# Optimization experiments

Hardware: AMD Instinct MI355X
Metric: run time of the kernel (lower is better)

## Reference

```python
import jax, jax.numpy as jnp
import numpy as np

B, C, H, W = 32, 128, 56, 56
O = 256
KH, KW = 3, 3
SH, SW = 1, 1
PH, PW = 1, 1
T = 6          # num_terms
R = 8          # low_rank
D = C * KH * KW          # 1152
R2 = R * KH * KW         # 72


def setup_inputs() -> dict:
    key = jax.random.key(0)
    ks = jax.random.split(key, 6)
    scale = 0.05
    return {
        "x": jax.random.normal(ks[0], (B, C, H, W), dtype=jnp.float32),
        "S1s": jax.random.normal(ks[1], (T, D, R), dtype=jnp.float32) * scale,
        "U1s": jax.random.normal(ks[2], (T, R, O), dtype=jnp.float32) * scale,
        "U2s": jax.random.normal(ks[3], (T, R2, D), dtype=jnp.float32) * scale,
        "S2s": jax.random.normal(ks[4], (T, R2, O), dtype=jnp.float32) * scale,
        "bias": jax.random.normal(ks[5], (O,), dtype=jnp.float32) * scale,
    }


def _extract_windows(x):
    # im2col: pad then gather strided windows; d flattened in (C, kh, kw) order
    xp = jnp.pad(x, ((0, 0), (0, 0), (PH, PH), (PW, PW)))
    Hp, Wp = xp.shape[2], xp.shape[3]
    Ho = (Hp - KH) // SH + 1
    Wo = (Wp - KW) // SW + 1
    # stack KH*KW shifted views -> [B, C, KH*KW, Ho, Wo]
    patches = jnp.stack(
        [xp[:, :, i:i + SH * Ho:SH, j:j + SW * Wo:SW]
         for i in range(KH) for j in range(KW)],
        axis=2,
    )
    # -> [B, Ho, Wo, C, KH*KW] -> [N, C*KH*KW]
    xw = patches.transpose(0, 3, 4, 1, 2).reshape(B * Ho * Wo, D)
    return xw, Ho, Wo


def reference(x, S1s, U1s, U2s, S2s, bias):
    xw, Ho, Wo = _extract_windows(x)                    # [N, D]
    # term 1: x_windows @ S1s[t] @ U1s[t], averaged over terms
    out1 = jnp.einsum('nd,tdr,tro->no', xw, S1s, U1s, optimize=True) / T + bias
    # term 2: x_windows @ U2s[t].T @ S2s[t], averaged over terms
    out2 = jnp.einsum('nd,tdr,tro->no', xw, jnp.swapaxes(U2s, 1, 2), S2s,
                      optimize=True) / T
    # NOTE: bias is added twice, faithfully matching the original module
    out = (out1 + out2 + bias).reshape(B, Ho, Wo, O).transpose(0, 3, 1, 2)
    return out
```

## Files before the change

### kernel.cpp

```cpp
#include <hip/hip_runtime.h>
#include <hip/hip_bf16.h>

typedef __attribute__((ext_vector_type(8))) short  short8;
typedef __attribute__((ext_vector_type(8))) unsigned short ushort8;
typedef __attribute__((ext_vector_type(4))) unsigned short usv4;
typedef __attribute__((ext_vector_type(4))) float  f32x4;

#define D_DIM 1152
#define O_DIM 256
#define N_TOT 100352
#define XT_H 58
#define XT_ROW (58 * 128)

__device__ __forceinline__ unsigned short f2bf(float f) {
  __hip_bfloat16 h = __float2bfloat16(f);
  return __builtin_bit_cast(unsigned short, h);
}

#define GLOAD_LDS16(g, l)                                              \
  __builtin_amdgcn_global_load_lds(                                    \
      (const __attribute__((address_space(1))) void*)(g),              \
      (__attribute__((address_space(3))) void*)(l), 16, 0, 0)

__global__ __launch_bounds__(256) void wt_kernel(
    const float* __restrict__ S1s, const float* __restrict__ U1s,
    const float* __restrict__ U2s, const float* __restrict__ S2s,
    unsigned short* __restrict__ Wt) {
  __shared__ float A_lds[32][64];
  __shared__ float B_lds[32][64];

  const int bo = blockIdx.x & 3;
  const int bd = blockIdx.x >> 2;
  const int o0  = bo << 6;
  const int dn0 = bd << 6;
  const int rr  = dn0 >> 7;
  const int c0  = dn0 & 127;

  const int tid = threadIdx.x;
  const int ty = tid >> 4, tx = tid & 15;

  float acc[4][4] = {};

  for (int kc = 0; kc < 15; ++kc) {
#pragma unroll
    for (int e = 0; e < 8; ++e) {
      const int li = e * 256 + tid;
      const int kk = li >> 6;
      const int xx = li & 63;
      const int k  = kc * 32 + kk;
      float av, bv;
      if (k < 48) {
        av = U1s[k * O_DIM + o0 + xx];
        const int d_old = (c0 + xx) * 9 + rr;
        bv = S1s[(size_t)((k >> 3) * D_DIM + d_old) * 8 + (k & 7)];
      } else {
        const int kq = k - 48;
        av = S2s[(size_t)kq * O_DIM + o0 + xx];
        const int d_old = (c0 + xx) * 9 + rr;
        bv = U2s[(size_t)kq * D_DIM + d_old];
      }
      A_lds[kk][xx] = av;
      B_lds[kk][xx] = bv;
    }
    __syncthreads();
#pragma unroll
    for (int kk = 0; kk < 32; ++kk) {
      f32x4 a = *(const f32x4*)&A_lds[kk][ty << 2];
      f32x4 b = *(const f32x4*)&B_lds[kk][tx << 2];
#pragma unroll
      for (int i = 0; i < 4; ++i)
#pragma unroll
        for (int j = 0; j < 4; ++j)
          acc[i][j] += a[i] * b[j];
    }
    __syncthreads();
  }

#pragma unroll
  for (int i = 0; i < 4; ++i) {
    usv4 v;
#pragma unroll
    for (int j = 0; j < 4; ++j) v[j] = f2bf(acc[i][j] * (1.0f / 6.0f));
    *(usv4*)(Wt + (size_t)(o0 + (ty << 2) + i) * D_DIM + dn0 + (tx << 2)) = v;
  }
}

__global__ __launch_bounds__(256) void pad_kernel(const float* __restrict__ x,
                                                  unsigned short* __restrict__ xt) {
  int blk = blockIdx.x;
  int b = blk / XT_H, ih = blk - b * XT_H;
  unsigned short* dst = xt + (size_t)blk * XT_ROW;
  int tid = threadIdx.x;

  if (ih == 0 || ih == XT_H - 1) {
    ushort8 z;
#pragma unroll
    for (int q = 0; q < 8; ++q) z[q] = 0;
    for (int i = tid; i < XT_ROW / 8; i += 256) ((ushort8*)dst)[i] = z;
    return;
  }

  __shared__ unsigned short lds[128 * 58];
  int h = ih - 1;
  const float* xb = x + (size_t)b * 128 * 3136 + (size_t)h * 56;
#pragma unroll 4
  for (int r = 0; r < 28; ++r) {
    int idx = r * 256 + tid;
    int c = idx / 56, w2 = idx - c * 56;
    lds[c * 58 + w2] = f2bf(xb[(size_t)c * 3136 + w2]);
  }
  __syncthreads();
#pragma unroll 4
  for (int r = 0; r < 29; ++r) {
    int idx = r * 256 + tid;
    int iw = idx >> 7, c = idx & 127;
    unsigned short v = 0;
    if (iw >= 1 && iw <= 56) v = lds[c * 58 + (iw - 1)];
    dst[idx] = v;
  }
}

__device__ __forceinline__ constexpr int KOF(int kt) {
  int rr = kt >> 1;
  return ((rr / 3) * 58 + (rr % 3)) * 128 + (kt & 1) * 64;
}

#define AFRAG(row_, ks_)                                                       \
  (*(const short8*)((const char*)smem + (row_) * 128 +                        \
      (((((ks_) << 2) + (lane >> 4)) ^ ((row_) & 7)) << 4)))
#define BFRAG(row_, ks_)                                                       \
  (*(const short8*)((const char*)smem + 16384 + (row_) * 128 +                \
      (((((ks_) << 2) + (lane >> 4)) ^ ((row_) & 7)) << 4)))

__global__ __launch_bounds__(256) void gemm_kernel(
    const unsigned short* __restrict__ Wt, const unsigned short* __restrict__ xt,
    const float* __restrict__ bias, float* __restrict__ out) {
  __shared__ __align__(1024) unsigned short smem[16384];

  const int bid   = blockIdx.x;
  const int lid   = (bid & 7) * 196 + (bid >> 3);
  const int ntile = lid >> 1, otile = lid & 1;
  const int n0 = ntile << 7, o0 = otile << 7;

  const int tid  = threadIdx.x;
  const int w    = tid >> 6;
  const int lane = tid & 63;
  const int wr   = (w >> 1) << 6;
  const int wc   = (w & 1) << 6;
  const int la15 = lane & 15;

  const unsigned short* pA[4];
  const unsigned short* pB[4];
#pragma unroll
  for (int j = 0; j < 4; ++j) {
    const int chunk = (w << 2) + j;
    const int row   = (chunk << 3) + (lane >> 3);
    const int gs    = (lane & 7) ^ (row & 7);
    pA[j] = Wt + (size_t)(o0 + row) * D_DIM + gs * 8;
    const int n_g = n0 + row;
    const int b   = n_g / 3136;
    const int s   = n_g - b * 3136;
    const int oh  = s / 56, ow = s - oh * 56;
    pB[j] = xt + (((size_t)b * XT_H + oh) * XT_H + ow) * 128 + gs * 8;
  }

  f32x4 acc[4][4] = {};

#pragma unroll
  for (int kt = 0; kt < 18; ++kt) {
    const int ka = kt << 6;
    const int kb = KOF(kt);
#pragma unroll
    for (int j = 0; j < 4; ++j) {
      const int chunk = (w << 2) + j;
      GLOAD_LDS16(pA[j] + ka, smem + (chunk << 9) + ((lane & 7) << 3) + ((lane >> 3) << 6));
      GLOAD_LDS16(pB[j] + kb, smem + 8192 + (chunk << 9) + ((lane & 7) << 3) + ((lane >> 3) << 6));
    }
    __syncthreads();

#pragma unroll
    for (int ks = 0; ks < 2; ++ks) {
      short8 af[4], bfr[4];
#pragma unroll
      for (int m = 0; m < 4; ++m)
        af[m] = AFRAG(wr + m * 16 + la15, ks);
#pragma unroll
      for (int n = 0; n < 4; ++n)
        bfr[n] = BFRAG(wc + n * 16 + la15, ks);
#pragma unroll
      for (int m = 0; m < 4; ++m)
#pragma unroll
        for (int n = 0; n < 4; ++n)
          acc[m][n] = __builtin_amdgcn_mfma_f32_16x16x32_bf16(af[m], bfr[n], acc[m][n], 0, 0, 0);
    }
    __syncthreads();
  }

  const int lr = (lane >> 4) << 2;
#pragma unroll
  for (int n = 0; n < 4; ++n) {
    const int ng = n0 + wc + n * 16 + la15;
    const int b  = ng / 3136;
    const int s  = ng - b * 3136;
    float* op = out + (size_t)b * (O_DIM * 3136) + s;
#pragma unroll
    for (int m = 0; m < 4; ++m) {
      const int og = o0 + wr + m * 16 + lr;
#pragma unroll
      for (int r = 0; r < 4; ++r)
        op[(size_t)(og + r) * 3136] = acc[m][n][r] + 2.0f * bias[og + r];
    }
  }
}

extern "C" void kernel_launch(void* const* d_in, const int* in_sizes, int n_in,
                              void* d_out, int out_size, void* d_ws, size_t ws_size,
                              hipStream_t stream) {
  const float* x    = (const float*)d_in[0];
  const float* S1s  = (const float*)d_in[1];
  const float* U1s  = (const float*)d_in[2];
  const float* U2s  = (const float*)d_in[3];
  const float* S2s  = (const float*)d_in[4];
  const float* bias = (const float*)d_in[5];
  float* out = (float*)d_out;
  (void)ws_size;

  unsigned short* xt = (unsigned short*)d_ws;
  unsigned short* Wt = (unsigned short*)((char*)d_ws + (size_t)32 * XT_H * XT_ROW * 2);

  pad_kernel<<<dim3(32 * XT_H), dim3(256), 0, stream>>>(x, xt);
  wt_kernel<<<dim3(72), dim3(256), 0, stream>>>(S1s, U1s, U2s, S2s, Wt);
  gemm_kernel<<<dim3(1568), dim3(256), 0, stream>>>(Wt, xt, bias, out);
}
```

Measured before the change: 124.7 us.

## Replace LDS-staged GEMM with register-direct global loads and 128x128 per-wave tiles

The GEMM kernel drops LDS staging through global_load_lds and barriers. Each wave now loads its MFMA fragments straight from global memory into registers and computes a 128x128 tile, with double-buffered register prefetch across 36 k-steps of 32. The block tile grows to 256x256 over 392 blocks, with one block per CU via launch bounds. This removes LDS traffic and syncs and raises arithmetic per wave. The cost is very high register pressure (64 accumulators plus 32 fragments), no data sharing between waves, and uncoalesced 16-byte global loads that depend on cache hits.

```diff
diff --git a/kernel.cpp b/kernel.cpp
--- a/kernel.cpp
+++ b/kernel.cpp
@@ -16,11 +16,6 @@
   __hip_bfloat16 h = __float2bfloat16(f);
   return __builtin_bit_cast(unsigned short, h);
 }
-
-#define GLOAD_LDS16(g, l)                                              \
-  __builtin_amdgcn_global_load_lds(                                    \
-      (const __attribute__((address_space(1))) void*)(g),              \
-      (__attribute__((address_space(3))) void*)(l), 16, 0, 0)
 
 __global__ __launch_bounds__(256) void wt_kernel(
     const float* __restrict__ S1s, const float* __restrict__ U1s,
@@ -120,95 +115,91 @@
   }
 }
 
-__device__ __forceinline__ constexpr int KOF(int kt) {
-  int rr = kt >> 1;
-  return ((rr / 3) * 58 + (rr % 3)) * 128 + (kt & 1) * 64;
-}
-
-#define AFRAG(row_, ks_)                                                       \
-  (*(const short8*)((const char*)smem + (row_) * 128 +                        \
-      (((((ks_) << 2) + (lane >> 4)) ^ ((row_) & 7)) << 4)))
-#define BFRAG(row_, ks_)                                                       \
-  (*(const short8*)((const char*)smem + 16384 + (row_) * 128 +                \
-      (((((ks_) << 2) + (lane >> 4)) ^ ((row_) & 7)) << 4)))
-
-__global__ __launch_bounds__(256) void gemm_kernel(
+__device__ __forceinline__ int koffB(int s) {
+  const int rr = s >> 2;
+  const int kh = (rr * 11) >> 5;
+  const int kw = rr - kh * 3;
+  return (kh * XT_H + kw) * 128 + (((s >> 1) & 1) << 6) + ((s & 1) << 5);
+}
+
+#define LOADA(dst, s_) do {                                                    \
+  const unsigned short* _pa = pA + (s_) * 32;                                  \
+  _Pragma("unroll")                                                            \
+  for (int mi = 0; mi < 8; ++mi)                                               \
+    dst[mi] = *(const short8*)(_pa + mi * (16 * D_DIM));                       \
+} while (0)
+
+#define LOADB(dst, s_) do {                                                    \
+  const int _kb = koffB(s_);                                                   \
+  _Pragma("unroll")                                                            \
+  for (int ni = 0; ni < 8; ++ni)                                               \
+    dst[ni] = *(const short8*)(pB[ni] + _kb);                                  \
+} while (0)
+
+#define MFMA_ALL(A_, B_) do {                                                  \
+  _Pragma("unroll")                                                            \
+  for (int mi = 0; mi < 8; ++mi)                                               \
+    _Pragma("unroll")                                                          \
+    for (int ni = 0; ni < 8; ++ni)                                             \
+      acc[mi][ni] = __builtin_amdgcn_mfma_f32_16x16x32_bf16(                   \
+          A_[mi], B_[ni], acc[mi][ni], 0, 0, 0);                               \
+} while (0)
+
+__global__ __launch_bounds__(256, 1) void gemm_kernel(
     const unsigned short* __restrict__ Wt, const unsigned short* __restrict__ xt,
     const float* __restrict__ bias, float* __restrict__ out) {
-  __shared__ __align__(1024) unsigned short smem[16384];
-
   const int bid   = blockIdx.x;
-  const int lid   = (bid & 7) * 196 + (bid >> 3);
-  const int ntile = lid >> 1, otile = lid & 1;
-  const int n0 = ntile << 7, o0 = otile << 7;
+  const int ntile = (bid & 7) * 49 + (bid >> 3);
+  const int n0    = ntile << 8;
 
   const int tid  = threadIdx.x;
+  const int lane = tid & 63;
   const int w    = tid >> 6;
-  const int lane = tid & 63;
-  const int wr   = (w >> 1) << 6;
-  const int wc   = (w & 1) << 6;
+  const int o_w  = (w >> 1) << 7;
+  const int n_w  = n0 + ((w & 1) << 7);
   const int la15 = lane & 15;
-
-  const unsigned short* pA[4];
-  const unsigned short* pB[4];
-#pragma unroll
-  for (int j = 0; j < 4; ++j) {
-    const int chunk = (w << 2) + j;
-    const int row   = (chunk << 3) + (lane >> 3);
-    const int gs    = (lane & 7) ^ (row & 7);
-    pA[j] = Wt + (size_t)(o0 + row) * D_DIM + gs * 8;
-    const int n_g = n0 + row;
+  const int kq8  = (lane >> 4) << 3;
+
+  const unsigned short* pA = Wt + (size_t)(o_w + la15) * D_DIM + kq8;
+  const unsigned short* pB[8];
+#pragma unroll
+  for (int ni = 0; ni < 8; ++ni) {
+    const int n_g = n_w + ni * 16 + la15;
     const int b   = n_g / 3136;
     const int s   = n_g - b * 3136;
     const int oh  = s / 56, ow = s - oh * 56;
-    pB[j] = xt + (((size_t)b * XT_H + oh) * XT_H + ow) * 128 + gs * 8;
-  }
-
-  f32x4 acc[4][4] = {};
-
-#pragma unroll
-  for (int kt = 0; kt < 18; ++kt) {
-    const int ka = kt << 6;
-    const int kb = KOF(kt);
-#pragma unroll
-    for (int j = 0; j < 4; ++j) {
-      const int chunk = (w << 2) + j;
-      GLOAD_LDS16(pA[j] + ka, smem + (chunk << 9) + ((lane & 7) << 3) + ((lane >> 3) << 6));
-      GLOAD_LDS16(pB[j] + kb, smem + 8192 + (chunk << 9) + ((lane & 7) << 3) + ((lane >> 3) << 6));
-    }
-    __syncthreads();
-
-#pragma unroll
-    for (int ks = 0; ks < 2; ++ks) {
-      short8 af[4], bfr[4];
-#pragma unroll
-      for (int m = 0; m < 4; ++m)
-        af[m] = AFRAG(wr + m * 16 + la15, ks);
-#pragma unroll
-      for (int n = 0; n < 4; ++n)
-        bfr[n] = BFRAG(wc + n * 16 + la15, ks);
-#pragma unroll
-      for (int m = 0; m < 4; ++m)
-#pragma unroll
-        for (int n = 0; n < 4; ++n)
-          acc[m][n] = __builtin_amdgcn_mfma_f32_16x16x32_bf16(af[m], bfr[n], acc[m][n], 0, 0, 0);
-    }
-    __syncthreads();
+    pB[ni] = xt + (((size_t)b * XT_H + oh) * XT_H + ow) * 128 + kq8;
+  }
+
+  f32x4 acc[8][8] = {};
+  short8 aP[8], bP[8], aQ[8], bQ[8];
+
+  LOADA(aP, 0);
+  LOADB(bP, 0);
+
+  for (int s = 0; s < 36; s += 2) {
+    LOADA(aQ, s + 1);
+    LOADB(bQ, s + 1);
+    MFMA_ALL(aP, bP);
+    const int s2 = (s + 2 < 36) ? s + 2 : 35;
+    LOADA(aP, s2);
+    LOADB(bP, s2);
+    MFMA_ALL(aQ, bQ);
   }
 
   const int lr = (lane >> 4) << 2;
 #pragma unroll
-  for (int n = 0; n < 4; ++n) {
-    const int ng = n0 + wc + n * 16 + la15;
+  for (int ni = 0; ni < 8; ++ni) {
+    const int ng = n_w + ni * 16 + la15;
     const int b  = ng / 3136;
     const int s  = ng - b * 3136;
     float* op = out + (size_t)b * (O_DIM * 3136) + s;
 #pragma unroll
-    for (int m = 0; m < 4; ++m) {
-      const int og = o0 + wr + m * 16 + lr;
+    for (int mi = 0; mi < 8; ++mi) {
+      const int og = o_w + mi * 16 + lr;
 #pragma unroll
       for (int r = 0; r < 4; ++r)
-        op[(size_t)(og + r) * 3136] = acc[m][n][r] + 2.0f * bias[og + r];
+        op[(size_t)(og + r) * 3136] = acc[mi][ni][r] + 2.0f * bias[og + r];
     }
   }
 }
@@ -230,5 +221,5 @@
 
   pad_kernel<<<dim3(32 * XT_H), dim3(256), 0, stream>>>(x, xt);
   wt_kernel<<<dim3(72), dim3(256), 0, stream>>>(S1s, U1s, U2s, S2s, Wt);
-  gemm_kernel<<<dim3(1568), dim3(256), 0, stream>>>(Wt, xt, bias, out);
-}
+  gemm_kernel<<<dim3(392), dim3(256), 0, stream>>>(Wt, xt, bias, out);
+}
```

After: 360.1 us. 189% more time.

## Double-buffer LDS in GEMM kernel to overlap global loads with MFMA

Applied to the files above, without the earlier changes.

Doubles the shared-memory staging area so the next K-tile is loaded via global_load_lds while the current tile's MFMAs run, with one barrier per iteration instead of two. All fragments for a tile are read up front and the MFMA block runs under raised wave priority. The cost is twice the LDS per block (64KB), which may reduce how many blocks fit on a CU. There is also a possible hazard: buffer bf^1 is overwritten while other waves may still be reading it, since the single barrier sits after the fragment reads.

```diff
diff --git a/kernel.cpp b/kernel.cpp
--- a/kernel.cpp
+++ b/kernel.cpp
@@ -125,17 +125,28 @@
   return ((rr / 3) * 58 + (rr % 3)) * 128 + (kt & 1) * 64;
 }
 
-#define AFRAG(row_, ks_)                                                       \
-  (*(const short8*)((const char*)smem + (row_) * 128 +                        \
+#define STAGE(kt_, bf_) do {                                                   \
+  _Pragma("unroll")                                                            \
+  for (int j = 0; j < 4; ++j) {                                                \
+    const int chunk = (w << 2) + j;                                            \
+    GLOAD_LDS16(pA[j] + (kt_) * 64,                                            \
+                smem + (bf_) * 16384 + (chunk << 9) + sdst);                   \
+    GLOAD_LDS16(pB[j] + KOF(kt_),                                              \
+                smem + (bf_) * 16384 + 8192 + (chunk << 9) + sdst);            \
+  }                                                                            \
+} while (0)
+
+#define AFRAG(bf_, row_, ks_)                                                  \
+  (*(const short8*)((const char*)smem + (bf_) * 32768 + (row_) * 128 +        \
       (((((ks_) << 2) + (lane >> 4)) ^ ((row_) & 7)) << 4)))
-#define BFRAG(row_, ks_)                                                       \
-  (*(const short8*)((const char*)smem + 16384 + (row_) * 128 +                \
+#define BFRAG(bf_, row_, ks_)                                                  \
+  (*(const short8*)((const char*)smem + (bf_) * 32768 + 16384 + (row_) * 128 +\
       (((((ks_) << 2) + (lane >> 4)) ^ ((row_) & 7)) << 4)))
 
 __global__ __launch_bounds__(256) void gemm_kernel(
     const unsigned short* __restrict__ Wt, const unsigned short* __restrict__ xt,
     const float* __restrict__ bias, float* __restrict__ out) {
-  __shared__ __align__(1024) unsigned short smem[16384];
+  __shared__ __align__(1024) unsigned short smem[32768];
 
   const int bid   = blockIdx.x;
   const int lid   = (bid & 7) * 196 + (bid >> 3);
@@ -148,6 +159,8 @@
   const int wr   = (w >> 1) << 6;
   const int wc   = (w & 1) << 6;
   const int la15 = lane & 15;
+
+  const int sdst = ((lane & 7) << 3) + ((lane >> 3) << 6);
 
   const unsigned short* pA[4];
   const unsigned short* pB[4];
@@ -166,34 +179,43 @@
 
   f32x4 acc[4][4] = {};
 
+  STAGE(0, 0);
+  asm volatile("s_waitcnt vmcnt(0)" ::: "memory");
+  __builtin_amdgcn_s_barrier();
+
 #pragma unroll
   for (int kt = 0; kt < 18; ++kt) {
-    const int ka = kt << 6;
-    const int kb = KOF(kt);
-#pragma unroll
-    for (int j = 0; j < 4; ++j) {
-      const int chunk = (w << 2) + j;
-      GLOAD_LDS16(pA[j] + ka, smem + (chunk << 9) + ((lane & 7) << 3) + ((lane >> 3) << 6));
-      GLOAD_LDS16(pB[j] + kb, smem + 8192 + (chunk << 9) + ((lane & 7) << 3) + ((lane >> 3) << 6));
-    }
-    __syncthreads();
-
-#pragma unroll
-    for (int ks = 0; ks < 2; ++ks) {
-      short8 af[4], bfr[4];
+    const int bf = kt & 1;
+
+    if (kt + 1 < 18) STAGE(kt + 1, bf ^ 1);
+
+    short8 af[4][2], bfr[4][2];
+#pragma unroll
+    for (int m = 0; m < 4; ++m) {
+      af[m][0] = AFRAG(bf, wr + m * 16 + la15, 0);
+      af[m][1] = AFRAG(bf, wr + m * 16 + la15, 1);
+    }
+#pragma unroll
+    for (int n = 0; n < 4; ++n) {
+      bfr[n][0] = BFRAG(bf, wc + n * 16 + la15, 0);
+      bfr[n][1] = BFRAG(bf, wc + n * 16 + la15, 1);
+    }
+
+    __builtin_amdgcn_s_setprio(1);
+#pragma unroll
+    for (int ks = 0; ks < 2; ++ks)
 #pragma unroll
       for (int m = 0; m < 4; ++m)
-        af[m] = AFRAG(wr + m * 16 + la15, ks);
-#pragma unroll
-      for (int n = 0; n < 4; ++n)
-        bfr[n] = BFRAG(wc + n * 16 + la15, ks);
-#pragma unroll
-      for (int m = 0; m < 4; ++m)
 #pragma unroll
         for (int n = 0; n < 4; ++n)
-          acc[m][n] = __builtin_amdgcn_mfma_f32_16x16x32_bf16(af[m], bfr[n], acc[m][n], 0, 0, 0);
-    }
-    __syncthreads();
+          acc[m][n] = __builtin_amdgcn_mfma_f32_16x16x32_bf16(
+              af[m][ks], bfr[n][ks], acc[m][n], 0, 0, 0);
+    __builtin_amdgcn_s_setprio(0);
+
+    if (kt + 1 < 18) {
+      asm volatile("s_waitcnt vmcnt(0)" ::: "memory");
+      __builtin_amdgcn_s_barrier();
+    }
   }
 
   const int lr = (lane >> 4) << 2;
```

Result: faster. 114.7 us, median of 2 (-8.0%).

## Double-buffer GEMM LDS stages with K=32 slices and prefetch next stage

Applied to the files above, without the earlier changes.

Restructures the GEMM main loop from 18 single-buffered K=64 tiles into 36 double-buffered K=32 stages. Each stage's global-to-LDS load is issued before the MFMAs on the current buffer, so one barrier per stage replaces two. The change also adjusts the swizzle for 64-byte rows, adds s_setprio around the MFMA block, and sets launch_bounds occupancy to 5. The risk is that smaller K slices double the barrier count and shorten the window for overlapping the prefetch.

```diff
diff --git a/kernel.cpp b/kernel.cpp
--- a/kernel.cpp
+++ b/kernel.cpp
@@ -120,19 +120,27 @@
   }
 }
 
-__device__ __forceinline__ constexpr int KOF(int kt) {
-  int rr = kt >> 1;
-  return ((rr / 3) * 58 + (rr % 3)) * 128 + (kt & 1) * 64;
-}
-
-#define AFRAG(row_, ks_)                                                       \
-  (*(const short8*)((const char*)smem + (row_) * 128 +                        \
-      (((((ks_) << 2) + (lane >> 4)) ^ ((row_) & 7)) << 4)))
-#define BFRAG(row_, ks_)                                                       \
-  (*(const short8*)((const char*)smem + 16384 + (row_) * 128 +                \
-      (((((ks_) << 2) + (lane >> 4)) ^ ((row_) & 7)) << 4)))
-
-__global__ __launch_bounds__(256) void gemm_kernel(
+__device__ __forceinline__ constexpr int KOFS(int s) {
+  int rr = s >> 2;
+  return ((rr / 3) * 58 + (rr % 3)) * 128 + (s & 3) * 32;
+}
+
+#define STAGE_S(s_) do {                                                       \
+  unsigned short* _d = smem + ((s_) & 1) * 8192 + (tid << 3);                  \
+  GLOAD_LDS16(pA[0] + (s_) * 32, _d);                                          \
+  GLOAD_LDS16(pA[1] + (s_) * 32, _d + 2048);                                   \
+  GLOAD_LDS16(pB[0] + KOFS(s_), _d + 4096);                                    \
+  GLOAD_LDS16(pB[1] + KOFS(s_), _d + 6144);                                    \
+} while (0)
+
+#define AFRAG(sl_, row_)                                                       \
+  (*(const short8*)((const char*)smem + (sl_) * 16384 + (row_) * 64 +         \
+      (((lane >> 4) ^ (((row_) >> 1) & 3)) << 4)))
+#define BFRAG(sl_, row_)                                                       \
+  (*(const short8*)((const char*)smem + (sl_) * 16384 + 8192 + (row_) * 64 +  \
+      (((lane >> 4) ^ (((row_) >> 1) & 3)) << 4)))
+
+__global__ __launch_bounds__(256, 5) void gemm_kernel(
     const unsigned short* __restrict__ Wt, const unsigned short* __restrict__ xt,
     const float* __restrict__ bias, float* __restrict__ out) {
   __shared__ __align__(1024) unsigned short smem[16384];
@@ -149,51 +157,53 @@
   const int wc   = (w & 1) << 6;
   const int la15 = lane & 15;
 
-  const unsigned short* pA[4];
-  const unsigned short* pB[4];
-#pragma unroll
-  for (int j = 0; j < 4; ++j) {
-    const int chunk = (w << 2) + j;
-    const int row   = (chunk << 3) + (lane >> 3);
-    const int gs    = (lane & 7) ^ (row & 7);
-    pA[j] = Wt + (size_t)(o0 + row) * D_DIM + gs * 8;
-    const int n_g = n0 + row;
+  const int srow = tid >> 2;
+  const int sg   = (tid & 3) ^ ((tid >> 3) & 3);
+  const unsigned short* pA[2];
+  const unsigned short* pB[2];
+#pragma unroll
+  for (int r = 0; r < 2; ++r) {
+    pA[r] = Wt + (size_t)(o0 + r * 64 + srow) * D_DIM + sg * 8;
+    const int n_g = n0 + r * 64 + srow;
     const int b   = n_g / 3136;
     const int s   = n_g - b * 3136;
     const int oh  = s / 56, ow = s - oh * 56;
-    pB[j] = xt + (((size_t)b * XT_H + oh) * XT_H + ow) * 128 + gs * 8;
+    pB[r] = xt + (((size_t)b * XT_H + oh) * XT_H + ow) * 128 + sg * 8;
   }
 
   f32x4 acc[4][4] = {};
 
-#pragma unroll
-  for (int kt = 0; kt < 18; ++kt) {
-    const int ka = kt << 6;
-    const int kb = KOF(kt);
-#pragma unroll
-    for (int j = 0; j < 4; ++j) {
-      const int chunk = (w << 2) + j;
-      GLOAD_LDS16(pA[j] + ka, smem + (chunk << 9) + ((lane & 7) << 3) + ((lane >> 3) << 6));
-      GLOAD_LDS16(pB[j] + kb, smem + 8192 + (chunk << 9) + ((lane & 7) << 3) + ((lane >> 3) << 6));
-    }
-    __syncthreads();
-
-#pragma unroll
-    for (int ks = 0; ks < 2; ++ks) {
-      short8 af[4], bfr[4];
-#pragma unroll
-      for (int m = 0; m < 4; ++m)
-        af[m] = AFRAG(wr + m * 16 + la15, ks);
+  STAGE_S(0);
+  asm volatile("s_waitcnt vmcnt(0)" ::: "memory");
+  __builtin_amdgcn_s_barrier();
+
+#pragma unroll
+  for (int s = 0; s < 36; ++s) {
+    const int sl = s & 1;
+
+    if (s + 1 < 36) STAGE_S(s + 1);
+
+    short8 af[4], bfr[4];
+#pragma unroll
+    for (int m = 0; m < 4; ++m)
+      af[m] = AFRAG(sl, wr + m * 16 + la15);
+#pragma unroll
+    for (int n = 0; n < 4; ++n)
+      bfr[n] = BFRAG(sl, wc + n * 16 + la15);
+
+    __builtin_amdgcn_s_setprio(1);
+#pragma unroll
+    for (int m = 0; m < 4; ++m)
 #pragma unroll
       for (int n = 0; n < 4; ++n)
-        bfr[n] = BFRAG(wc + n * 16 + la15, ks);
-#pragma unroll
-      for (int m = 0; m < 4; ++m)
-#pragma unroll
-        for (int n = 0; n < 4; ++n)
-          acc[m][n] = __builtin_amdgcn_mfma_f32_16x16x32_bf16(af[m], bfr[n], acc[m][n], 0, 0, 0);
-    }
-    __syncthreads();
+        acc[m][n] = __builtin_amdgcn_mfma_f32_16x16x32_bf16(
+            af[m], bfr[n], acc[m][n], 0, 0, 0);
+    __builtin_amdgcn_s_setprio(0);
+
+    if (s + 1 < 36) {
+      asm volatile("s_waitcnt vmcnt(0)" ::: "memory");
+      __builtin_amdgcn_s_barrier();
+    }
   }
 
   const int lr = (lane >> 4) << 2;
```

Result: slower. 299.3 us (+140.0%).
